# Kernel tuning notes

Measured on AMD Instinct MI355X. Metric: run time of the kernel, lower is better.

The kernel has to match this reference:

```python
import jax, jax.numpy as jnp
import numpy as np

B, S, D = 4, 2048, 1024
H = 16
DH = D // H  # dim_q = dim_k = 64
F = 4096
EPS = 1e-5


def setup_inputs() -> dict:
    key = jax.random.key(0)
    ks = jax.random.split(key, 16)
    sd = 0.02
    inp = {
        'x': jax.random.normal(ks[0], (B, S, D), jnp.float32),
        'wq': jax.random.normal(ks[1], (H, D, DH), jnp.float32) * sd,
        'bq': jnp.zeros((H, DH), jnp.float32),
        'wk': jax.random.normal(ks[2], (H, D, DH), jnp.float32) * sd,
        'bk': jnp.zeros((H, DH), jnp.float32),
        'wv': jax.random.normal(ks[3], (H, D, DH), jnp.float32) * sd,
        'bv': jnp.zeros((H, DH), jnp.float32),
        'wo': jax.random.normal(ks[4], (H * DH, D), jnp.float32) * sd,
        'bo': jnp.zeros((D,), jnp.float32),
        'ln1_g': jnp.ones((D,), jnp.float32),
        'ln1_b': jnp.zeros((D,), jnp.float32),
        'w1': jax.random.normal(ks[5], (D, F), jnp.float32) * sd,
        'b1': jnp.zeros((F,), jnp.float32),
        'w2': jax.random.normal(ks[6], (F, D), jnp.float32) * sd,
        'b2': jnp.zeros((D,), jnp.float32),
        'ln2_g': jnp.ones((D,), jnp.float32),
        'ln2_b': jnp.zeros((D,), jnp.float32),
    }
    return inp


def _layernorm(x, g, b):
    mu = jnp.mean(x, axis=-1, keepdims=True)
    var = jnp.mean(jnp.square(x - mu), axis=-1, keepdims=True)
    return (x - mu) * jax.lax.rsqrt(var + EPS) * g + b


def _encoder_layer(x, wq, bq, wk, bk, wv, bv, wo, bo, ln1_g, ln1_b,
                   w1, b1, w2, b2, ln2_g, ln2_b):
    # Multi-head attention (all heads batched via einsum)
    q = jnp.einsum('bsd,hde->bhse', x, wq) + bq[:, None, :]
    k = jnp.einsum('bsd,hde->bhse', x, wk) + bk[:, None, :]
    v = jnp.einsum('bsd,hde->bhse', x, wv) + bv[:, None, :]
    scores = jnp.einsum('bhqe,bhke->bhqk', q, k) / jnp.sqrt(jnp.float32(DH))
    p = jax.nn.softmax(scores, axis=-1)
    o = jnp.einsum('bhqk,bhke->bhqe', p, v)  # [B,H,S,DH]
    o = o.transpose(0, 2, 1, 3).reshape(B, S, H * DH)  # concat heads
    attn = o @ wo + bo
    y = _layernorm(x + attn, ln1_g, ln1_b)  # post-norm residual
    # Feed-forward
    ff = jax.nn.relu(y @ w1 + b1) @ w2 + b2
    return _layernorm(y + ff, ln2_g, ln2_b)


def reference(x, wq, bq, wk, bk, wv, bv, wo, bo, ln1_g, ln1_b,
              w1, b1, w2, b2, ln2_g, ln2_b):
    return _encoder_layer(x, wq, bq, wk, bk, wv, bv, wo, bo, ln1_g, ln1_b,
                          w1, b1, w2, b2, ln2_g, ln2_b)
```

## Files before the change

### kernel.cpp

```cpp
#include <hip/hip_runtime.h>
#include <stdint.h>


typedef short bf16x8 __attribute__((ext_vector_type(8)));
typedef unsigned short u16x8 __attribute__((ext_vector_type(8)));
typedef float f32x4 __attribute__((ext_vector_type(4)));
typedef unsigned int u32x2 __attribute__((ext_vector_type(2)));

#define MFMA16(a, b, c) __builtin_amdgcn_mfma_f32_16x16x32_bf16((a), (b), (c), 0, 0, 0)

#define QSCALE 0.1803368801111204f

__device__ __forceinline__ float b2f(unsigned short u) {
    union { unsigned u32; float f; } x;
    x.u32 = ((unsigned)u) << 16;
    return x.f;
}
__device__ __forceinline__ unsigned short f2b(float f) {
    union { float f; unsigned u; } x;
    x.f = f;
    unsigned r = x.u + 0x7fff + ((x.u >> 16) & 1);
    return (unsigned short)(r >> 16);
}
__device__ __forceinline__ unsigned pack2(float lo, float hi) {
    union { float f; unsigned u; } a, b;
    a.f = lo; b.f = hi;
    return __builtin_amdgcn_perm(b.u + 0x8000u, a.u + 0x8000u, 0x07060302u);
}

__device__ __forceinline__ void gl16(const unsigned short* g, unsigned short* l) {
    __builtin_amdgcn_global_load_lds(
        (__attribute__((address_space(1))) unsigned int*)(unsigned long)g,
        (__attribute__((address_space(3))) unsigned int*)l, 16, 0, 0);
}

__global__ __launch_bounds__(256) void f2b_bulk(const float* __restrict__ in,
                                                unsigned short* __restrict__ out) {
    const long i = ((long)blockIdx.x * 256 + threadIdx.x) * 8;
    float4 a = *(const float4*)&in[i];
    float4 b = *(const float4*)&in[i + 4];
    u16x8 u;
    u[0] = f2b(a.x); u[1] = f2b(a.y); u[2] = f2b(a.z); u[3] = f2b(a.w);
    u[4] = f2b(b.x); u[5] = f2b(b.y); u[6] = f2b(b.z); u[7] = f2b(b.w);
    *(u16x8*)&out[i] = u;
}

__global__ void transpose_f2b(const float* __restrict__ in,
                              unsigned short* __restrict__ out,
                              int R, int C, long in_batch_stride,
                              int out_row0, int out_ld) {
    __shared__ float tile[32][33];
    const int batch = blockIdx.z;
    const float* src = in + (long)batch * in_batch_stride;
    const int c0 = blockIdx.x * 32, r0 = blockIdx.y * 32;
    const int tx = threadIdx.x, ty = threadIdx.y;
#pragma unroll
    for (int i = 0; i < 32; i += 8)
        tile[ty + i][tx] = src[(long)(r0 + ty + i) * C + c0 + tx];
    __syncthreads();
#pragma unroll
    for (int i = 0; i < 32; i += 8)
        out[(long)(out_row0 + batch * C + c0 + ty + i) * out_ld + r0 + tx] =
            f2b(tile[tx][ty + i]);
}

__global__ void transpose_v(const unsigned short* __restrict__ qkv,
                            unsigned short* __restrict__ vt) {
    __shared__ unsigned short tile[32][33];
    const int bh = blockIdx.z;
    const int b = bh >> 4, h = bh & 15;
    const int s0 = blockIdx.x * 32, e0 = blockIdx.y * 32;
    const int tx = threadIdx.x, ty = threadIdx.y;
    const unsigned short* src = qkv + ((long)b * 2048) * 3072 + 2048 + h * 64;
#pragma unroll
    for (int i = 0; i < 32; i += 8)
        tile[ty + i][tx] = src[(long)(s0 + ty + i) * 3072 + e0 + tx];
    __syncthreads();
    unsigned short* dst = vt + ((long)bh * 64) * 2048;
#pragma unroll
    for (int i = 0; i < 32; i += 8)
        dst[(long)(e0 + ty + i) * 2048 + s0 + tx] = tile[tx][ty + i];
}

__global__ void concat_bias(const float* __restrict__ bq,
                            const float* __restrict__ bk,
                            const float* __restrict__ bv,
                            float* __restrict__ out) {
    int n = blockIdx.x * 256 + threadIdx.x;
    out[n] = (n < 1024) ? bq[n] : (n < 2048) ? bk[n - 1024] : bv[n - 2048];
}

__device__ __forceinline__ float to_f(float v) { return v; }
__device__ __forceinline__ float to_f(unsigned short v) { return b2f(v); }

template <typename RT>
__global__ __launch_bounds__(256) void gemm_bt(
    const unsigned short* __restrict__ A, const unsigned short* __restrict__ Bt,
    unsigned short* __restrict__ C, const float* __restrict__ bias,
    const RT* __restrict__ resid, int M, int N, int K, int op) {
    __shared__ __align__(16) unsigned short As[2 * 128 * 32];
    __shared__ __align__(16) unsigned short Bs[2 * 128 * 32];
    const int tid = threadIdx.x;
    const int wave = tid >> 6, lane = tid & 63;
    const int quad = lane >> 4, lr = lane & 15;
    const int wm = (wave >> 1) << 6, wn = (wave & 1) << 6;
    const long m0 = (long)blockIdx.y * 128;
    const long n0 = (long)blockIdx.x * 128;

    f32x4 acc[4][4] = {};

    const int srow = wave * 32 + (lane >> 2);
    const int scol = (lane & 3) * 8;
    const unsigned short* ga = A + (m0 + srow) * (long)K + scol;
    const unsigned short* gb = Bt + (n0 + srow) * (long)K + scol;
    unsigned short* la = &As[wave * 32 * 32];
    unsigned short* lb = &Bs[wave * 32 * 32];
    const long rstep = 16 * (long)K;

    for (int k0 = 0; k0 < K; k0 += 64) {
        gl16(ga + k0, la);
        gl16(ga + k0 + rstep, la + 512);
        gl16(ga + k0 + 32, la + 4096);
        gl16(ga + k0 + 32 + rstep, la + 4096 + 512);
        gl16(gb + k0, lb);
        gl16(gb + k0 + rstep, lb + 512);
        gl16(gb + k0 + 32, lb + 4096);
        gl16(gb + k0 + 32 + rstep, lb + 4096 + 512);
        __syncthreads();
#pragma unroll
        for (int kh = 0; kh < 2; kh++) {
            const int kb = kh * 4096;
            bf16x8 af[4], bfr[4];
#pragma unroll
            for (int mi = 0; mi < 4; mi++)
                af[mi] = *(const bf16x8*)&As[kb + (wm + mi * 16 + lr) * 32 + quad * 8];
#pragma unroll
            for (int ni = 0; ni < 4; ni++)
                bfr[ni] = *(const bf16x8*)&Bs[kb + (wn + ni * 16 + lr) * 32 + quad * 8];
#pragma unroll
            for (int mi = 0; mi < 4; mi++)
#pragma unroll
                for (int ni = 0; ni < 4; ni++)
                    acc[mi][ni] = MFMA16(af[mi], bfr[ni], acc[mi][ni]);
        }
        __syncthreads();
    }

#pragma unroll
    for (int ni = 0; ni < 4; ni++) {
        const long col = n0 + wn + ni * 16 + lr;
        const float bv = bias ? bias[col] : 0.0f;
        const float cscale = (op == 2 && col < 1024) ? QSCALE : 1.0f;
#pragma unroll
        for (int mi = 0; mi < 4; mi++) {
#pragma unroll
            for (int r = 0; r < 4; r++) {
                const long row = m0 + wm + mi * 16 + quad * 4 + r;
                float v = (acc[mi][ni][r] + bv) * cscale;
                if (resid) v += to_f(resid[row * (long)N + col]);
                if (op == 1) v = fmaxf(v, 0.0f);
                C[row * (long)N + col] = f2b(v);
            }
        }
    }
}

__global__ __launch_bounds__(256, 5) void attn_kernel(
    const unsigned short* __restrict__ qkv, const unsigned short* __restrict__ vt,
    unsigned short* __restrict__ o) {
    __shared__ __align__(16) unsigned short Klds[2][64 * 64];
    __shared__ __align__(16) unsigned short Vlds[2][64 * 64];
    const int l = blockIdx.x;
    const int bh = ((l >> 8) << 3) | (l & 7);
    const int qt = (l >> 3) & 31;
    const int b = bh >> 4, h = bh & 15;
    const int tid = threadIdx.x;
    const int wave = tid >> 6, lane = tid & 63;
    const int quad = lane >> 4, lr = lane & 15;
    const long rowbase = (long)b * 2048;
    const int qb = qt * 64 + wave * 16;

    bf16x8 q0, q1;
    {
        const unsigned short* qrow = qkv + (rowbase + qb + lr) * 3072 + h * 64;
        q0 = *(const bf16x8*)&qrow[quad * 8];
        q1 = *(const bf16x8*)&qrow[32 + quad * 8];
    }

    bf16x8 ones;
#pragma unroll
    for (int i = 0; i < 8; i++) ones[i] = (short)0x3F80;

    const int srow = lane >> 3;
    const int sxc = (lane & 7) ^ srow;
    const unsigned short* kp =
        qkv + (rowbase + wave * 16 + srow) * 3072 + 1024 + h * 64 + sxc * 8;
    const unsigned short* vp =
        vt + ((long)bh * 64 + wave * 16 + srow) * 2048 + sxc * 8;
    const long KADV = 64L * 3072;
    unsigned short* const kd0 = &Klds[0][wave * 16 * 64];
    unsigned short* const vd0 = &Vlds[0][wave * 16 * 64];

#define STAGE(bf)                                                     \
    {                                                                 \
        gl16(kp, kd0 + (bf)*4096);                                    \
        gl16(kp + 8 * 3072, kd0 + (bf)*4096 + 8 * 64);                \
        gl16(vp, vd0 + (bf)*4096);                                    \
        gl16(vp + 8 * 2048, vd0 + (bf)*4096 + 8 * 64);                \
    }

    f32x4 oacc[4] = {};
    f32x4 dacc = {};

    const int x7 = lr & 7;
    const int c00 = (quad ^ x7) * 8;
    const int c01 = ((4 | quad) ^ x7) * 8;

    STAGE(0);
    __syncthreads();

    for (int kt = 0; kt < 32; kt++) {
        const int buf = kt & 1;
        if (kt < 31) {
            kp += KADV;
            vp += 64;
            STAGE(buf ^ 1);
        }
        const unsigned short* kb = &Klds[buf][0];
        f32x4 s4[4];
#pragma unroll
        for (int nt = 0; nt < 4; nt++) {
            const unsigned short* krow = kb + (nt * 16 + lr) * 64;
            bf16x8 k0 = *(const bf16x8*)&krow[c00];
            bf16x8 k1 = *(const bf16x8*)&krow[c01];
            f32x4 z = {};
            z = MFMA16(k0, q0, z);
            z = MFMA16(k1, q1, z);
            s4[nt] = z;
        }
        unsigned pwv[4][2];
#pragma unroll
        for (int nt = 0; nt < 4; nt++) {
            float p0 = exp2f(s4[nt][0]);
            float p1 = exp2f(s4[nt][1]);
            float p2 = exp2f(s4[nt][2]);
            float p3 = exp2f(s4[nt][3]);
            asm("v_cvt_pk_bf16_f32 %0, %1, %2"
                : "=v"(pwv[nt][0]) : "v"(p0), "v"(p1));
            asm("v_cvt_pk_bf16_f32 %0, %1, %2"
                : "=v"(pwv[nt][1]) : "v"(p2), "v"(p3));
        }
        unsigned pq[2][4];
#pragma unroll
        for (int kc = 0; kc < 2; kc++)
#pragma unroll
            for (int tl = 0; tl < 2; tl++) {
                u32x2 y = __builtin_amdgcn_permlane32_swap(
                    pwv[2 * kc][tl], pwv[2 * kc + 1][tl], false, false);
                u32x2 z = __builtin_amdgcn_permlane16_swap(y[0], y[1], false, false);
                pq[kc][tl] = z[0];
                pq[kc][2 + tl] = z[1];
            }

        const unsigned short* vb = &Vlds[buf][0];
#pragma unroll
        for (int kc = 0; kc < 2; kc++) {
            union { unsigned u[4]; bf16x8 h; } pu;
            pu.u[0] = pq[kc][0]; pu.u[1] = pq[kc][1];
            pu.u[2] = pq[kc][2]; pu.u[3] = pq[kc][3];
            const int vc = kc ? c01 : c00;
            dacc = MFMA16(ones, pu.h, dacc);
#pragma unroll
            for (int nt = 0; nt < 4; nt++) {
                bf16x8 va = *(const bf16x8*)&vb[(nt * 16 + lr) * 64 + vc];
                oacc[nt] = MFMA16(va, pu.h, oacc[nt]);
            }
        }
        __syncthreads();
    }

    const float rinv = 1.0f / dacc[0];

    const long orow = rowbase + qb + lr;
#pragma unroll
    for (int nt = 0; nt < 4; nt++) {
        ushort4 ov = {f2b(oacc[nt][0] * rinv), f2b(oacc[nt][1] * rinv),
                      f2b(oacc[nt][2] * rinv), f2b(oacc[nt][3] * rinv)};
        *(ushort4*)&o[orow * 1024 + h * 64 + nt * 16 + quad * 4] = ov;
    }
#undef STAGE
}

__device__ __forceinline__ void st4(float* p, float a, float b, float c, float d) {
    float4 v = {a, b, c, d};
    *(float4*)p = v;
}
__device__ __forceinline__ void st4(unsigned short* p, float a, float b, float c,
                                    float d) {
    ushort4 v = {f2b(a), f2b(b), f2b(c), f2b(d)};
    *(ushort4*)p = v;
}

template <typename OT>
__global__ __launch_bounds__(256) void ln_kernel(
    const unsigned short* __restrict__ in, const float* __restrict__ g,
    const float* __restrict__ b, OT* __restrict__ out) {
    __shared__ float red[4];
    const long row = blockIdx.x;
    const int tid = threadIdx.x;
    ushort4 u = *(const ushort4*)&in[row * 1024 + tid * 4];
    float v[4] = {b2f(u.x), b2f(u.y), b2f(u.z), b2f(u.w)};
    float s = v[0] + v[1] + v[2] + v[3];
#pragma unroll
    for (int off = 32; off > 0; off >>= 1) s += __shfl_down(s, off, 64);
    if ((tid & 63) == 0) red[tid >> 6] = s;
    __syncthreads();
    const float mu = (red[0] + red[1] + red[2] + red[3]) * (1.0f / 1024.0f);
    __syncthreads();
    float d[4], sq = 0.f;
#pragma unroll
    for (int i = 0; i < 4; i++) { d[i] = v[i] - mu; sq += d[i] * d[i]; }
#pragma unroll
    for (int off = 32; off > 0; off >>= 1) sq += __shfl_down(sq, off, 64);
    if ((tid & 63) == 0) red[tid >> 6] = sq;
    __syncthreads();
    const float var = (red[0] + red[1] + red[2] + red[3]) * (1.0f / 1024.0f);
    const float rs = rsqrtf(var + 1e-5f);
    float4 gu = *(const float4*)&g[tid * 4];
    float4 bu = *(const float4*)&b[tid * 4];
    st4(&out[row * 1024 + tid * 4], d[0] * rs * gu.x + bu.x,
        d[1] * rs * gu.y + bu.y, d[2] * rs * gu.z + bu.z,
        d[3] * rs * gu.w + bu.w);
}

extern "C" void kernel_launch(void* const* d_in, const int* in_sizes, int n_in,
                              void* d_out, int out_size, void* d_ws, size_t ws_size,
                              hipStream_t stream) {
    (void)in_sizes; (void)n_in; (void)out_size; (void)ws_size;
    const float* x   = (const float*)d_in[0];
    const float* wq  = (const float*)d_in[1];
    const float* bq  = (const float*)d_in[2];
    const float* wk  = (const float*)d_in[3];
    const float* bk  = (const float*)d_in[4];
    const float* wv  = (const float*)d_in[5];
    const float* bv  = (const float*)d_in[6];
    const float* wo  = (const float*)d_in[7];
    const float* bo  = (const float*)d_in[8];
    const float* g1  = (const float*)d_in[9];
    const float* be1 = (const float*)d_in[10];
    const float* w1  = (const float*)d_in[11];
    const float* b1  = (const float*)d_in[12];
    const float* w2  = (const float*)d_in[13];
    const float* b2  = (const float*)d_in[14];
    const float* g2  = (const float*)d_in[15];
    const float* be2 = (const float*)d_in[16];

    char* ws = (char*)d_ws;
    const size_t MB = 1024 * 1024;
    unsigned short* WT_QKV = (unsigned short*)(ws + 0);
    unsigned short* WT_O   = (unsigned short*)(ws + 6 * MB);
    unsigned short* WT_1   = (unsigned short*)(ws + 8 * MB);
    unsigned short* WT_2   = (unsigned short*)(ws + 16 * MB);
    float*          BQKV   = (float*)(ws + 24 * MB);
    unsigned short* XB     = (unsigned short*)(ws + 25 * MB);
    unsigned short* QKV    = (unsigned short*)(ws + 41 * MB);
    unsigned short* O      = (unsigned short*)(ws + 89 * MB);
    unsigned short* R1     = (unsigned short*)(ws + 25 * MB);
    unsigned short* Y      = (unsigned short*)(ws + 41 * MB);
    unsigned short* R2     = (unsigned short*)(ws + 57 * MB);
    unsigned short* Hb     = (unsigned short*)(ws + 73 * MB);
    unsigned short* VT     = (unsigned short*)(ws + 137 * MB);
    float*          OUT    = (float*)d_out;

    const dim3 tb(32, 8, 1);
    transpose_f2b<<<dim3(2, 32, 16), tb, 0, stream>>>(wq, WT_QKV, 1024, 64, 65536L, 0, 1024);
    transpose_f2b<<<dim3(2, 32, 16), tb, 0, stream>>>(wk, WT_QKV, 1024, 64, 65536L, 1024, 1024);
    transpose_f2b<<<dim3(2, 32, 16), tb, 0, stream>>>(wv, WT_QKV, 1024, 64, 65536L, 2048, 1024);
    transpose_f2b<<<dim3(32, 32, 1), tb, 0, stream>>>(wo, WT_O, 1024, 1024, 0L, 0, 1024);
    transpose_f2b<<<dim3(128, 32, 1), tb, 0, stream>>>(w1, WT_1, 1024, 4096, 0L, 0, 1024);
    transpose_f2b<<<dim3(32, 128, 1), tb, 0, stream>>>(w2, WT_2, 4096, 1024, 0L, 0, 4096);
    concat_bias<<<dim3(12), 256, 0, stream>>>(bq, bk, bv, BQKV);
    f2b_bulk<<<dim3(4096), 256, 0, stream>>>(x, XB);

    gemm_bt<unsigned short><<<dim3(24, 64), 256, 0, stream>>>(
        XB, WT_QKV, QKV, BQKV, (const unsigned short*)nullptr, 8192, 3072, 1024, 2);
    transpose_v<<<dim3(64, 2, 64), tb, 0, stream>>>(QKV, VT);
    attn_kernel<<<dim3(2048), 256, 0, stream>>>(QKV, VT, O);
    gemm_bt<float><<<dim3(8, 64), 256, 0, stream>>>(
        O, WT_O, R1, bo, x, 8192, 1024, 1024, 0);
    ln_kernel<unsigned short><<<dim3(8192), 256, 0, stream>>>(R1, g1, be1, Y);
    gemm_bt<unsigned short><<<dim3(32, 64), 256, 0, stream>>>(
        Y, WT_1, Hb, b1, (const unsigned short*)nullptr, 8192, 4096, 1024, 1);
    gemm_bt<unsigned short><<<dim3(8, 64), 256, 0, stream>>>(
        Hb, WT_2, R2, b2, Y, 8192, 1024, 4096, 0);
    ln_kernel<float><<<dim3(8192), 256, 0, stream>>>(R2, g2, be2, OUT);
}
```

Before: 611.6 us.

## Replace GEMM with 4-stage LDS ring pipeline, 256x128 tiles and XCD-aware block swizzle

The GEMM kernel becomes a 512-thread, 256x128-tile kernel that keeps a 4-slot LDS ring of 32-wide K stages. Loads are issued three stages ahead and gated by explicit vmcnt waits with a single barrier per stage, replacing the old load-sync-compute-sync loop. Block indices are remapped so consecutive tiles land on the same XCD, which should improve L2 reuse. This is meant to hide global-load latency and cut synchronisation, at the cost of more LDS (96KB) and a hand-managed wait count that relies on exact load ordering.

```diff
diff --git a/kernel.cpp b/kernel.cpp
--- a/kernel.cpp
+++ b/kernel.cpp
@@ -21,11 +21,6 @@
     x.f = f;
     unsigned r = x.u + 0x7fff + ((x.u >> 16) & 1);
     return (unsigned short)(r >> 16);
-}
-__device__ __forceinline__ unsigned pack2(float lo, float hi) {
-    union { float f; unsigned u; } a, b;
-    a.f = lo; b.f = hi;
-    return __builtin_amdgcn_perm(b.u + 0x8000u, a.u + 0x8000u, 0x07060302u);
 }
 
 __device__ __forceinline__ void gl16(const unsigned short* g, unsigned short* l) {
@@ -94,68 +89,84 @@
 __device__ __forceinline__ float to_f(unsigned short v) { return b2f(v); }
 
 template <typename RT>
-__global__ __launch_bounds__(256) void gemm_bt(
+__global__ __launch_bounds__(512, 2) void gemm_ring(
     const unsigned short* __restrict__ A, const unsigned short* __restrict__ Bt,
     unsigned short* __restrict__ C, const float* __restrict__ bias,
     const RT* __restrict__ resid, int M, int N, int K, int op) {
-    __shared__ __align__(16) unsigned short As[2 * 128 * 32];
-    __shared__ __align__(16) unsigned short Bs[2 * 128 * 32];
+    __shared__ __align__(16) unsigned short As[4][256 * 32];
+    __shared__ __align__(16) unsigned short Bs[4][128 * 32];
     const int tid = threadIdx.x;
     const int wave = tid >> 6, lane = tid & 63;
     const int quad = lane >> 4, lr = lane & 15;
-    const int wm = (wave >> 1) << 6, wn = (wave & 1) << 6;
-    const long m0 = (long)blockIdx.y * 128;
-    const long n0 = (long)blockIdx.x * 128;
+    const int wm = wave >> 1, wn = wave & 1;
+
+    const int nwg = gridDim.x * gridDim.y;
+    const int orig = blockIdx.y * gridDim.x + blockIdx.x;
+    const int wg = (orig & 7) * (nwg >> 3) + (orig >> 3);
+    const long n0 = (long)(wg % gridDim.x) * 128;
+    const long m0 = (long)(wg / gridDim.x) * 256;
 
     f32x4 acc[4][4] = {};
 
-    const int srow = wave * 32 + (lane >> 2);
-    const int scol = (lane & 3) * 8;
-    const unsigned short* ga = A + (m0 + srow) * (long)K + scol;
-    const unsigned short* gb = Bt + (n0 + srow) * (long)K + scol;
-    unsigned short* la = &As[wave * 32 * 32];
-    unsigned short* lb = &Bs[wave * 32 * 32];
+    const unsigned short* gA =
+        A + (m0 + wave * 32 + (lane >> 2)) * (long)K + (lane & 3) * 8;
+    const unsigned short* gB =
+        Bt + (n0 + wave * 16 + (lane >> 2)) * (long)K + (lane & 3) * 8;
     const long rstep = 16 * (long)K;
-
-    for (int k0 = 0; k0 < K; k0 += 64) {
-        gl16(ga + k0, la);
-        gl16(ga + k0 + rstep, la + 512);
-        gl16(ga + k0 + 32, la + 4096);
-        gl16(ga + k0 + 32 + rstep, la + 4096 + 512);
-        gl16(gb + k0, lb);
-        gl16(gb + k0 + rstep, lb + 512);
-        gl16(gb + k0 + 32, lb + 4096);
-        gl16(gb + k0 + 32 + rstep, lb + 4096 + 512);
-        __syncthreads();
-#pragma unroll
-        for (int kh = 0; kh < 2; kh++) {
-            const int kb = kh * 4096;
-            bf16x8 af[4], bfr[4];
-#pragma unroll
-            for (int mi = 0; mi < 4; mi++)
-                af[mi] = *(const bf16x8*)&As[kb + (wm + mi * 16 + lr) * 32 + quad * 8];
+    unsigned short* const lA0 = &As[0][wave * 32 * 32];
+    unsigned short* const lA1 = &As[0][(wave * 32 + 16) * 32];
+    unsigned short* const lB0 = &Bs[0][wave * 16 * 32];
+
+#define RSTAGE(si)                                                  \
+    {                                                               \
+        const int _sl = (si) & 3;                                   \
+        const long _kc = (long)(si) * 32;                           \
+        gl16(gA + _kc, lA0 + _sl * 8192);                           \
+        gl16(gA + rstep + _kc, lA1 + _sl * 8192);                   \
+        gl16(gB + _kc, lB0 + _sl * 4096);                           \
+    }
+
+    const int S = K >> 5;
+    RSTAGE(0);
+    RSTAGE(1);
+    RSTAGE(2);
+
+    for (int s = 0; s < S; ++s) {
+        if (s + 2 < S) {
+            asm volatile("s_waitcnt vmcnt(6)" ::: "memory");
+        } else if (s + 1 < S) {
+            asm volatile("s_waitcnt vmcnt(3)" ::: "memory");
+        } else {
+            asm volatile("s_waitcnt vmcnt(0)" ::: "memory");
+        }
+        __builtin_amdgcn_s_barrier();
+        const int slot = s & 3;
+        bf16x8 af[4], bfr[4];
+#pragma unroll
+        for (int mi = 0; mi < 4; mi++)
+            af[mi] = *(const bf16x8*)&As[slot][(wm * 64 + mi * 16 + lr) * 32 + quad * 8];
+#pragma unroll
+        for (int ni = 0; ni < 4; ni++)
+            bfr[ni] = *(const bf16x8*)&Bs[slot][(wn * 64 + ni * 16 + lr) * 32 + quad * 8];
+#pragma unroll
+        for (int mi = 0; mi < 4; mi++)
 #pragma unroll
             for (int ni = 0; ni < 4; ni++)
-                bfr[ni] = *(const bf16x8*)&Bs[kb + (wn + ni * 16 + lr) * 32 + quad * 8];
-#pragma unroll
-            for (int mi = 0; mi < 4; mi++)
-#pragma unroll
-                for (int ni = 0; ni < 4; ni++)
-                    acc[mi][ni] = MFMA16(af[mi], bfr[ni], acc[mi][ni]);
-        }
-        __syncthreads();
-    }
+                acc[mi][ni] = MFMA16(af[mi], bfr[ni], acc[mi][ni]);
+        if (s + 3 < S) RSTAGE(s + 3);
+    }
+#undef RSTAGE
 
 #pragma unroll
     for (int ni = 0; ni < 4; ni++) {
-        const long col = n0 + wn + ni * 16 + lr;
+        const long col = n0 + wn * 64 + ni * 16 + lr;
         const float bv = bias ? bias[col] : 0.0f;
         const float cscale = (op == 2 && col < 1024) ? QSCALE : 1.0f;
 #pragma unroll
         for (int mi = 0; mi < 4; mi++) {
 #pragma unroll
             for (int r = 0; r < 4; r++) {
-                const long row = m0 + wm + mi * 16 + quad * 4 + r;
+                const long row = m0 + wm * 64 + mi * 16 + quad * 4 + r;
                 float v = (acc[mi][ni][r] + bv) * cscale;
                 if (resid) v += to_f(resid[row * (long)N + col]);
                 if (op == 1) v = fmaxf(v, 0.0f);
@@ -382,16 +393,16 @@
     concat_bias<<<dim3(12), 256, 0, stream>>>(bq, bk, bv, BQKV);
     f2b_bulk<<<dim3(4096), 256, 0, stream>>>(x, XB);
 
-    gemm_bt<unsigned short><<<dim3(24, 64), 256, 0, stream>>>(
+    gemm_ring<unsigned short><<<dim3(24, 32), 512, 0, stream>>>(
         XB, WT_QKV, QKV, BQKV, (const unsigned short*)nullptr, 8192, 3072, 1024, 2);
     transpose_v<<<dim3(64, 2, 64), tb, 0, stream>>>(QKV, VT);
     attn_kernel<<<dim3(2048), 256, 0, stream>>>(QKV, VT, O);
-    gemm_bt<float><<<dim3(8, 64), 256, 0, stream>>>(
+    gemm_ring<float><<<dim3(8, 32), 512, 0, stream>>>(
         O, WT_O, R1, bo, x, 8192, 1024, 1024, 0);
     ln_kernel<unsigned short><<<dim3(8192), 256, 0, stream>>>(R1, g1, be1, Y);
-    gemm_bt<unsigned short><<<dim3(32, 64), 256, 0, stream>>>(
+    gemm_ring<unsigned short><<<dim3(32, 32), 512, 0, stream>>>(
         Y, WT_1, Hb, b1, (const unsigned short*)nullptr, 8192, 4096, 1024, 1);
-    gemm_bt<unsigned short><<<dim3(8, 64), 256, 0, stream>>>(
+    gemm_ring<unsigned short><<<dim3(8, 32), 512, 0, stream>>>(
         Hb, WT_2, R2, b2, Y, 8192, 1024, 4096, 0);
     ln_kernel<float><<<dim3(8192), 256, 0, stream>>>(R2, g2, be2, OUT);
 }
```

New measurement: 613.4 us. About the same (+0.3%).
